# Kernel optimization log

Hardware: AMD Instinct MI355X
Metric: run time of the kernel (lower is better)

The kernel has to match this reference:

```python
import jax, jax.numpy as jnp
import numpy as np

D_MODEL = 2048
NUM_HEADS = 16
NUM_KV_HEADS = 4
HEAD_DIM = D_MODEL // NUM_HEADS  # 128
ROPE_THETA = 10000.0
BATCH = 2
SEQ = 2048


def _rotate_half(x):
    # interleaved rotate-half: pairs (x0,x1) -> (-x1, x0)
    x1 = x[..., ::2]
    x2 = x[..., 1::2]
    return jnp.stack((-x2, x1), axis=-1).reshape(x.shape)


def _rope_tables(seq_len, dtype, start_pos=0):
    inv_freq = 1.0 / (ROPE_THETA ** (jnp.arange(0, HEAD_DIM, 2, dtype=jnp.float32) / HEAD_DIM))
    positions = jnp.arange(start_pos, start_pos + seq_len, dtype=jnp.float32)
    freqs = jnp.outer(positions, inv_freq)              # [S, HD/2]
    emb = jnp.repeat(freqs, 2, axis=-1)                  # [S, HD]
    cos = jnp.cos(emb).astype(dtype)[None, None, :, :]   # [1,1,S,HD]
    sin = jnp.sin(emb).astype(dtype)[None, None, :, :]
    return cos, sin


def setup_inputs() -> dict:
    key = jax.random.key(0)
    ks = jax.random.split(key, 5)
    s = 0.02
    x = jax.random.normal(ks[0], (BATCH, SEQ, D_MODEL), dtype=jnp.float32)
    wq = jax.random.normal(ks[1], (D_MODEL, NUM_HEADS * HEAD_DIM), dtype=jnp.float32) * s
    wk = jax.random.normal(ks[2], (D_MODEL, NUM_KV_HEADS * HEAD_DIM), dtype=jnp.float32) * s
    wv = jax.random.normal(ks[3], (D_MODEL, NUM_KV_HEADS * HEAD_DIM), dtype=jnp.float32) * s
    wo = jax.random.normal(ks[4], (D_MODEL, D_MODEL), dtype=jnp.float32) * s
    return {"x": x, "wq": wq, "wk": wk, "wv": wv, "wo": wo}


def reference(x, wq, wk, wv, wo):
    batch, seq_len, _ = x.shape
    # projections (bias-free linears)
    q = (x @ wq).reshape(batch, seq_len, NUM_HEADS, HEAD_DIM).transpose(0, 2, 1, 3)
    k = (x @ wk).reshape(batch, seq_len, NUM_KV_HEADS, HEAD_DIM).transpose(0, 2, 1, 3)
    v = (x @ wv).reshape(batch, seq_len, NUM_KV_HEADS, HEAD_DIM).transpose(0, 2, 1, 3)
    # RoPE
    cos, sin = _rope_tables(seq_len, q.dtype)
    q = q * cos + _rotate_half(q) * sin
    k = k * cos + _rotate_half(k) * sin
    # GQA: duplicate KV heads
    repeats = NUM_HEADS // NUM_KV_HEADS
    k = jnp.repeat(k, repeats, axis=1)
    v = jnp.repeat(v, repeats, axis=1)
    # causal SDPA
    scale = HEAD_DIM ** -0.5
    scores = jnp.einsum('bhqd,bhkd->bhqk', q, k) * scale
    causal = jnp.tril(jnp.ones((seq_len, seq_len), dtype=bool))
    scores = jnp.where(causal[None, None, :, :], scores, -jnp.inf)
    weights = jax.nn.softmax(scores, axis=-1)
    y = jnp.einsum('bhqk,bhkd->bhqd', weights, v)
    y = y.transpose(0, 2, 1, 3).reshape(batch, seq_len, NUM_HEADS * HEAD_DIM)
    return y @ wo
```

## Files before the change

### kernel.cpp

```cpp
#include <hip/hip_runtime.h>
#include <cstdint>
#include <cstddef>

using short8 = __attribute__((ext_vector_type(8))) short;
using f32x4  = __attribute__((ext_vector_type(4))) float;
using u16x4  = __attribute__((ext_vector_type(4))) unsigned short;

#define DEV __device__ __forceinline__

DEV unsigned short f2bf(float f) {
  unsigned int u = __builtin_bit_cast(unsigned int, f);
  u += 0x7fffu + ((u >> 16) & 1u);
  return (unsigned short)(u >> 16);
}
DEV float bf2f(unsigned short h) {
  unsigned int u = ((unsigned int)h) << 16;
  return __builtin_bit_cast(float, u);
}
DEV unsigned int cvtpk_bf16(float lo, float hi) {
  unsigned int d;
  asm("v_cvt_pk_bf16_f32 %0, %1, %2" : "=v"(d) : "v"(lo), "v"(hi));
  return d;
}

#define GLL16(gp, lp)                                                          \
  __builtin_amdgcn_global_load_lds(                                            \
      (const __attribute__((address_space(1))) char*)(const char*)(gp),        \
      (__attribute__((address_space(3))) char*)(char*)(lp), 16, 0, 0)

constexpr int BATCH = 2, SEQ = 2048, DMODEL = 2048, NH = 16, NKVH = 4, DH = 128;
constexpr int MROWS = BATCH * SEQ;
constexpr int NQKV  = DMODEL + 2 * NKVH * DH;
constexpr int KOFF  = DMODEL;
constexpr int VOFF  = DMODEL + NKVH * DH;
constexpr float SM_L2 = 0.12751388158f;


__global__ void k_prep(const float* __restrict__ x, unsigned short* __restrict__ xb,
                       float* __restrict__ tc, float* __restrict__ ts) {
  int id = blockIdx.x * 256 + threadIdx.x;
  if (id < SEQ * 64) {
    int pos = id >> 6, i = id & 63;
    float freq = __expf(-(float)i * 0.14391157f);
    float ang = (float)pos * freq;
    tc[id] = cosf(ang);
    ts[id] = sinf(ang);
  }
  float4 v = ((const float4*)x)[id];
  u16x4 o = { f2bf(v.x), f2bf(v.y), f2bf(v.z), f2bf(v.w) };
  ((u16x4*)xb)[id] = o;
}

__global__ __launch_bounds__(256) void k_wtrans4(
    const float* __restrict__ wq, const float* __restrict__ wk,
    const float* __restrict__ wv, const float* __restrict__ wo,
    unsigned short* __restrict__ wT, unsigned short* __restrict__ woT) {
  __shared__ float tile[32][33];
  const int z = blockIdx.z;
  const float* src; unsigned short* dst; int N;
  if (z == 0)      { src = wq; dst = wT;                        N = 2048; }
  else if (z == 1) { src = wo; dst = woT;                       N = 2048; }
  else if (z == 2) { src = wk; dst = wT + (size_t)KOFF * 2048;  N = 512; }
  else             { src = wv; dst = wT + (size_t)VOFF * 2048;  N = 512; }
  int n0 = blockIdx.x * 32, k0 = blockIdx.y * 32;
  if (n0 >= N) return;
  int tx = threadIdx.x, ty = threadIdx.y;
  #pragma unroll
  for (int r = ty; r < 32; r += 8)
    tile[r][tx] = src[(size_t)(k0 + r) * N + n0 + tx];
  __syncthreads();
  #pragma unroll
  for (int r = ty; r < 32; r += 8)
    dst[(size_t)(n0 + r) * 2048 + k0 + tx] = f2bf(tile[tx][r]);
}

__global__ __launch_bounds__(256) void k_vtrans(const unsigned short* __restrict__ qkv,
                                                unsigned short* __restrict__ vt) {
  __shared__ unsigned short tile[32][33];
  int s0 = blockIdx.x * 32, d0 = blockIdx.y * 32;
  int bk = blockIdx.z;
  const unsigned short* src = qkv + (size_t)(bk >> 2) * SEQ * NQKV + VOFF + (bk & 3) * DH;
  unsigned short* dst = vt + ((size_t)bk * DH + d0) * SEQ + s0;
  int tx = threadIdx.x, ty = threadIdx.y;
  #pragma unroll
  for (int r = ty; r < 32; r += 8)
    tile[r][tx] = src[(size_t)(s0 + r) * NQKV + d0 + tx];
  __syncthreads();
  #pragma unroll
  for (int r = ty; r < 32; r += 8)
    dst[(size_t)r * SEQ + tx] = tile[tx][r];
}


template <int BNT, bool OUTF32, bool ROPE>
__global__ __launch_bounds__(512, 2) void k_gemm256(
    const unsigned short* __restrict__ A,
    const unsigned short* __restrict__ Bt,
    void* __restrict__ C, int M, int N, int K,
    const float* __restrict__ tc, const float* __restrict__ ts) {
  constexpr int NF = BNT / 64;
  __shared__ unsigned short As[2][256 * 64];
  __shared__ unsigned short Bs[2][BNT * 64];

  const int t = threadIdx.x, l = t & 63, w = t >> 6;
  const int rl = l & 15, kg = l >> 4;
  const int wm = w >> 2, wn = w & 3;

  const int gx = gridDim.x;
  const int nwg = gx * gridDim.y;
  const int idl = blockIdx.y * gx + blockIdx.x;
  const int swz = (idl & 7) * (nwg >> 3) + (idl >> 3);
  const int m0 = (swz / gx) * 256, n0 = (swz % gx) * BNT;

  const unsigned short* aSrc[4];
  const unsigned short* bSrc[NF];
  #pragma unroll
  for (int i = 0; i < 4; ++i) {
    int c = i * 512 + t, row = c >> 3, q = c & 7;
    aSrc[i] = A + (size_t)(m0 + row) * K + ((q ^ (row & 7)) << 3);
  }
  #pragma unroll
  for (int i = 0; i < NF; ++i) {
    int c = i * 512 + t, row = c >> 3, q = c & 7;
    bSrc[i] = Bt + (size_t)(n0 + row) * K + ((q ^ (row & 7)) << 3);
  }

  f32x4 acc[8][NF] = {};

  const int nk = K / 64;
  #pragma unroll
  for (int i = 0; i < 4; ++i) GLL16(aSrc[i], (char*)As[0] + i * 8192 + t * 16);
  #pragma unroll
  for (int i = 0; i < NF; ++i) GLL16(bSrc[i], (char*)Bs[0] + i * 8192 + t * 16);

  int cur = 0;
  for (int kt = 0; kt < nk; ++kt) {
    if (kt + 1 < nk) {
      const int off = (kt + 1) * 64;
      #pragma unroll
      for (int i = 0; i < 4; ++i)
        GLL16(aSrc[i] + off, (char*)As[cur ^ 1] + i * 8192 + t * 16);
      #pragma unroll
      for (int i = 0; i < NF; ++i)
        GLL16(bSrc[i] + off, (char*)Bs[cur ^ 1] + i * 8192 + t * 16);
      if constexpr (NF == 4)      asm volatile("s_waitcnt vmcnt(8)" ::: "memory");
      else if constexpr (NF == 3) asm volatile("s_waitcnt vmcnt(7)" ::: "memory");
      else                        asm volatile("s_waitcnt vmcnt(6)" ::: "memory");
    } else {
      asm volatile("s_waitcnt vmcnt(0)" ::: "memory");
    }
    __builtin_amdgcn_sched_barrier(0);
    __builtin_amdgcn_s_barrier();

    const unsigned short* a = As[cur];
    const unsigned short* b = Bs[cur];
    auto rdA = [&](int mf, int ks) {
      int row = wm * 128 + mf * 16 + rl;
      return *(const short8*)&a[row * 64 + (((ks * 4 + kg) ^ (row & 7)) << 3)];
    };
    auto rdB = [&](int nf, int ks) {
      int row = wn * (BNT / 4) + nf * 16 + rl;
      return *(const short8*)&b[row * 64 + (((ks * 4 + kg) ^ (row & 7)) << 3)];
    };

    short8 aF[4][2], bF[NF][2];
    #pragma unroll
    for (int mi = 0; mi < 4; ++mi)
      #pragma unroll
      for (int ks = 0; ks < 2; ++ks) aF[mi][ks] = rdA(mi, ks);
    #pragma unroll
    for (int j = 0; j < NF; ++j) {
      #pragma unroll
      for (int ks = 0; ks < 2; ++ks) bF[j][ks] = rdB(j, ks);
      __builtin_amdgcn_s_setprio(1);
      #pragma unroll
      for (int mi = 0; mi < 4; ++mi)
        #pragma unroll
        for (int ks = 0; ks < 2; ++ks)
          acc[mi][j] = __builtin_amdgcn_mfma_f32_16x16x32_bf16(aF[mi][ks], bF[j][ks], acc[mi][j], 0, 0, 0);
      __builtin_amdgcn_s_setprio(0);
    }
    #pragma unroll
    for (int mi = 0; mi < 4; ++mi)
      #pragma unroll
      for (int ks = 0; ks < 2; ++ks) aF[mi][ks] = rdA(4 + mi, ks);
    #pragma unroll
    for (int j = 0; j < NF; ++j) {
      __builtin_amdgcn_s_setprio(1);
      #pragma unroll
      for (int mi = 0; mi < 4; ++mi)
        #pragma unroll
        for (int ks = 0; ks < 2; ++ks)
          acc[4 + mi][j] = __builtin_amdgcn_mfma_f32_16x16x32_bf16(aF[mi][ks], bF[j][ks], acc[4 + mi][j], 0, 0, 0);
      __builtin_amdgcn_s_setprio(0);
    }

    __builtin_amdgcn_s_barrier();
    cur ^= 1;
  }

  #pragma unroll
  for (int mf = 0; mf < 8; ++mf) {
    #pragma unroll
    for (int nf = 0; nf < NF; ++nf) {
      const int row0 = m0 + wm * 128 + mf * 16 + kg * 4;
      const int colb = n0 + wn * (BNT / 4) + nf * 16;
      const int col = colb + rl;
      if constexpr (ROPE) {
        if (colb < VOFF) {
          const int dd = (col & 127) >> 1;
          const float sgn = (col & 1) ? 1.0f : -1.0f;
          const float qs = (colb < KOFF) ? SM_L2 : 1.0f;
          #pragma unroll
          for (int r = 0; r < 4; ++r) {
            const int s = (row0 + r) & (SEQ - 1);
            const float c = tc[s * 64 + dd], sn = ts[s * 64 + dd];
            const float xv = acc[mf][nf][r];
            const float xp = __shfl_xor(xv, 1);
            acc[mf][nf][r] = (xv * c + sgn * xp * sn) * qs;
          }
        }
      }
      #pragma unroll
      for (int r = 0; r < 4; ++r) {
        if constexpr (OUTF32)
          ((float*)C)[(size_t)(row0 + r) * N + col] = acc[mf][nf][r];
        else
          ((unsigned short*)C)[(size_t)(row0 + r) * N + col] = f2bf(acc[mf][nf][r]);
      }
    }
  }
}


constexpr int QB = 128, KB = 64;
constexpr float THR = 8.0f;

__global__ __launch_bounds__(512, 4) void k_attn(const unsigned short* __restrict__ qkv,
                                                 const unsigned short* __restrict__ vt,
                                                 unsigned short* __restrict__ obuf) {
  __shared__ unsigned short Ks[2][KB * DH];
  __shared__ unsigned short Vs[2][DH * KB];
  __shared__ unsigned short Pw[8][16 * 64];

  const int t = threadIdx.x, l = t & 63, w = t >> 6;
  const int rl = l & 15, kg = l >> 4;

  const int id = blockIdx.x;
  const int b = id >> 8;
  const int u = id & 255;
  const int h = u >> 4;
  const int qtr = u & 15;
  const int qt = b ? (15 - qtr) : qtr;
  const int q0 = qt * QB;
  const int kvh = h >> 2;

  const unsigned short* qbase = qkv + (size_t)b * SEQ * NQKV;
  const unsigned short* kbase = qbase + KOFF + kvh * DH;
  const unsigned short* vtb = vt + (size_t)(b * NKVH + kvh) * DH * SEQ;

  const unsigned short* kp[2];
  const unsigned short* vp[2];
  #pragma unroll
  for (int i = 0; i < 2; ++i) {
    int c = i * 512 + t;
    int krow = c >> 4, kq = c & 15;
    kp[i] = kbase + (size_t)krow * NQKV + ((kq ^ (krow & 7)) << 3);
    int vrow = c >> 3, vq = c & 7;
    vp[i] = vtb + (size_t)vrow * SEQ + ((vq ^ (vrow & 7)) << 3);
  }

  const int qw0 = q0 + w * 16;

  short8 qF[4];
  {
    const size_t qr = (size_t)(qw0 + rl) * NQKV + h * DH;
    #pragma unroll
    for (int ks = 0; ks < 4; ++ks)
      qF[ks] = *(const short8*)(qbase + qr + ks * 32 + kg * 8);
  }

  f32x4 Oc[8] = {};
  float mr = -3e38f, lr = 0.f;

  char* pwB = (char*)Pw[w] + rl * 128;
  const int pkey = (rl & 7) << 4;
  const int nt = q0 / KB + 2;

  #pragma unroll
  for (int i = 0; i < 2; ++i) {
    GLL16(kp[i], (char*)Ks[0] + w * 1024 + i * 8192);
    GLL16(vp[i], (char*)Vs[0] + w * 1024 + i * 8192);
  }

  int cur = 0;
  for (int tt = 0; tt < nt; ++tt) {
    const int kv0 = tt * KB;
    const bool more = (tt + 1 < nt);
    if (more) {
      #pragma unroll
      for (int i = 0; i < 2; ++i) {
        GLL16(kp[i] + (size_t)(kv0 + KB) * NQKV, (char*)Ks[cur ^ 1] + w * 1024 + i * 8192);
        GLL16(vp[i] + (kv0 + KB),               (char*)Vs[cur ^ 1] + w * 1024 + i * 8192);
      }
      asm volatile("s_waitcnt vmcnt(4)" ::: "memory");
    } else {
      asm volatile("s_waitcnt vmcnt(0)" ::: "memory");
    }
    __builtin_amdgcn_sched_barrier(0);
    __builtin_amdgcn_s_barrier();

    if (kv0 < qw0 + 16) {
      const unsigned short* KsC = Ks[cur];
      const unsigned short* VsC = Vs[cur];

      f32x4 St[4] = {};
      __builtin_amdgcn_s_setprio(1);
      #pragma unroll
      for (int n = 0; n < 4; ++n) {
        const int kr = n * 16 + rl;
        #pragma unroll
        for (int ks = 0; ks < 4; ++ks) {
          short8 kF = *(const short8*)&KsC[kr * DH + (((ks * 4 + kg) ^ (kr & 7)) << 3)];
          St[n] = __builtin_amdgcn_mfma_f32_16x16x32_bf16(kF, qF[ks], St[n], 0, 0, 0);
        }
      }
      __builtin_amdgcn_s_setprio(0);

      float mx = -3e38f;
      const bool diag = (kv0 + KB - 1) > qw0;
      if (diag) {
        const int thr = qw0 + rl - kv0;
        #pragma unroll
        for (int n = 0; n < 4; ++n)
          #pragma unroll
          for (int r = 0; r < 4; ++r) {
            float s = St[n][r];
            if (n * 16 + kg * 4 + r > thr) s = -3e38f;
            St[n][r] = s;
            mx = fmaxf(mx, s);
          }
      } else {
        #pragma unroll
        for (int n = 0; n < 4; ++n)
          #pragma unroll
          for (int r = 0; r < 4; ++r) mx = fmaxf(mx, St[n][r]);
      }
      mx = fmaxf(mx, __shfl_xor(mx, 16));
      mx = fmaxf(mx, __shfl_xor(mx, 32));

      if (__any(mx > mr + THR)) {
        const float mnew = fmaxf(mr, mx);
        const float sf = exp2f(mr - mnew);
        mr = mnew;
        lr *= sf;
        float sfv[4];
        #pragma unroll
        for (int r = 0; r < 4; ++r) sfv[r] = __shfl(sf, kg * 4 + r, 16);
        #pragma unroll
        for (int c = 0; c < 8; ++c)
          #pragma unroll
          for (int r = 0; r < 4; ++r) Oc[c][r] *= sfv[r];
      }

      float rs = 0.f;
      #pragma unroll
      for (int n = 0; n < 4; ++n) {
        float e0 = exp2f(St[n][0] - mr);
        float e1 = exp2f(St[n][1] - mr);
        float e2 = exp2f(St[n][2] - mr);
        float e3 = exp2f(St[n][3] - mr);
        rs += (e0 + e1) + (e2 + e3);
        uint2 d;
        d.x = cvtpk_bf16(e0, e1);
        d.y = cvtpk_bf16(e2, e3);
        *(uint2*)(pwB + ((n * 32 + kg * 8) ^ pkey)) = d;
      }
      rs += __shfl_xor(rs, 16);
      rs += __shfl_xor(rs, 32);
      lr += rs;

      short8 pF[2];
      #pragma unroll
      for (int ks2 = 0; ks2 < 2; ++ks2)
        pF[ks2] = *(const short8*)(pwB + ((ks2 * 64 + kg * 16) ^ pkey));
      __builtin_amdgcn_s_setprio(1);
      #pragma unroll
      for (int c = 0; c < 8; ++c) {
        const int vr = c * 16 + rl;
        #pragma unroll
        for (int ks2 = 0; ks2 < 2; ++ks2) {
          short8 vF = *(const short8*)&VsC[vr * KB + (((ks2 * 4 + kg) ^ (vr & 7)) << 3)];
          Oc[c] = __builtin_amdgcn_mfma_f32_16x16x32_bf16(pF[ks2], vF, Oc[c], 0, 0, 0);
        }
      }
      __builtin_amdgcn_s_setprio(0);
    }

    __builtin_amdgcn_s_barrier();
    cur ^= 1;
  }

  const float linv = 1.0f / lr;
  float inv[4];
  #pragma unroll
  for (int r = 0; r < 4; ++r) inv[r] = __shfl(linv, kg * 4 + r, 16);
  #pragma unroll
  for (int c = 0; c < 8; ++c)
    #pragma unroll
    for (int r = 0; r < 4; ++r) {
      int row = b * SEQ + qw0 + kg * 4 + r;
      obuf[(size_t)row * DMODEL + h * DH + c * 16 + rl] = f2bf(Oc[c][r] * inv[r]);
    }
}


extern "C" void kernel_launch(void* const* d_in, const int* in_sizes, int n_in,
                              void* d_out, int out_size, void* d_ws, size_t ws_size,
                              hipStream_t stream) {
  const float* x  = (const float*)d_in[0];
  const float* wq = (const float*)d_in[1];
  const float* wk = (const float*)d_in[2];
  const float* wv = (const float*)d_in[3];
  const float* wo = (const float*)d_in[4];
  float* out = (float*)d_out;

  unsigned short* xb  = (unsigned short*)d_ws;
  unsigned short* wT  = xb  + (size_t)MROWS * DMODEL;
  unsigned short* woT = wT  + (size_t)NQKV * DMODEL;
  unsigned short* qkv = woT + (size_t)DMODEL * DMODEL;
  unsigned short* ob  = qkv + (size_t)MROWS * NQKV;
  float* tc = (float*)(ob + (size_t)MROWS * DMODEL);
  float* ts = tc + SEQ * 64;
  unsigned short* vtG = wT;

  k_prep<<<dim3(MROWS * DMODEL / 4 / 256), dim3(256), 0, stream>>>(x, xb, tc, ts);
  k_wtrans4<<<dim3(64, 64, 4), dim3(32, 8), 0, stream>>>(wq, wk, wv, wo, wT, woT);

  k_gemm256<192, false, true><<<dim3(NQKV / 192, MROWS / 256), dim3(512), 0, stream>>>(
      xb, wT, qkv, MROWS, NQKV, DMODEL, tc, ts);
  k_vtrans<<<dim3(SEQ / 32, DH / 32, BATCH * NKVH), dim3(32, 8), 0, stream>>>(qkv, vtG);
  k_attn<<<dim3(512), dim3(512), 0, stream>>>(qkv, vtG, ob);
  k_gemm256<128, true, false><<<dim3(DMODEL / 128, MROWS / 256), dim3(512), 0, stream>>>(
      ob, woT, out, MROWS, DMODEL, DMODEL, nullptr, nullptr);
}
```

Baseline: 212.3 us.

## Switch attention to 32x32x16 MFMA with register-resident P via permlane32 swap

Reworks the attention inner loop to use 32x32x16 bf16 MFMAs. Each pair of waves now shares a 32-row query tile, and each wave in the pair computes one 64-wide half of the head dimension. The softmax probabilities stay in registers and are rearranged with v_permlane32_swap into the B-operand layout, so the per-wave LDS scratch buffer and its write/read round-trip are removed. Scale factors become per-lane and the output is stored as packed 4-element bf16 writes. In exchange, the QK^T scores are computed twice (once by each wave in a pair), and the larger fragments raise register pressure under the 512x4 launch bounds.

```diff
diff --git a/kernel.cpp b/kernel.cpp
--- a/kernel.cpp
+++ b/kernel.cpp
@@ -4,6 +4,7 @@
 
 using short8 = __attribute__((ext_vector_type(8))) short;
 using f32x4  = __attribute__((ext_vector_type(4))) float;
+using f32x16 = __attribute__((ext_vector_type(16))) float;
 using u16x4  = __attribute__((ext_vector_type(4))) unsigned short;
 
 #define DEV __device__ __forceinline__
@@ -241,10 +242,12 @@
                                                  unsigned short* __restrict__ obuf) {
   __shared__ unsigned short Ks[2][KB * DH];
   __shared__ unsigned short Vs[2][DH * KB];
-  __shared__ unsigned short Pw[8][16 * 64];
 
   const int t = threadIdx.x, l = t & 63, w = t >> 6;
-  const int rl = l & 15, kg = l >> 4;
+  const int ql = l & 31;
+  const int hi = l >> 5;
+  const int wq = w >> 1;
+  const int dhalf = (w & 1) * 64;
 
   const int id = blockIdx.x;
   const int b = id >> 8;
@@ -270,21 +273,19 @@
     vp[i] = vtb + (size_t)vrow * SEQ + ((vq ^ (vrow & 7)) << 3);
   }
 
-  const int qw0 = q0 + w * 16;
-
-  short8 qF[4];
+  const int qw0 = q0 + wq * 32;
+
+  short8 qF[8];
   {
-    const size_t qr = (size_t)(qw0 + rl) * NQKV + h * DH;
-    #pragma unroll
-    for (int ks = 0; ks < 4; ++ks)
-      qF[ks] = *(const short8*)(qbase + qr + ks * 32 + kg * 8);
-  }
-
-  f32x4 Oc[8] = {};
+    const size_t qr = (size_t)(qw0 + ql) * NQKV + h * DH;
+    #pragma unroll
+    for (int ks = 0; ks < 8; ++ks)
+      qF[ks] = *(const short8*)(qbase + qr + ks * 16 + hi * 8);
+  }
+
+  f32x16 Oc[2] = {};
   float mr = -3e38f, lr = 0.f;
 
-  char* pwB = (char*)Pw[w] + rl * 128;
-  const int pkey = (rl & 7) << 4;
   const int nt = q0 / KB + 2;
 
   #pragma unroll
@@ -310,19 +311,19 @@
     __builtin_amdgcn_sched_barrier(0);
     __builtin_amdgcn_s_barrier();
 
-    if (kv0 < qw0 + 16) {
+    if (kv0 < qw0 + 32) {
       const unsigned short* KsC = Ks[cur];
       const unsigned short* VsC = Vs[cur];
 
-      f32x4 St[4] = {};
+      f32x16 St[2] = {};
       __builtin_amdgcn_s_setprio(1);
       #pragma unroll
-      for (int n = 0; n < 4; ++n) {
-        const int kr = n * 16 + rl;
-        #pragma unroll
-        for (int ks = 0; ks < 4; ++ks) {
-          short8 kF = *(const short8*)&KsC[kr * DH + (((ks * 4 + kg) ^ (kr & 7)) << 3)];
-          St[n] = __builtin_amdgcn_mfma_f32_16x16x32_bf16(kF, qF[ks], St[n], 0, 0, 0);
+      for (int c = 0; c < 2; ++c) {
+        const int krow = c * 32 + ql;
+        #pragma unroll
+        for (int ks = 0; ks < 8; ++ks) {
+          short8 kF = *(const short8*)&KsC[krow * DH + (((ks * 2 + hi) ^ (krow & 7)) << 3)];
+          St[c] = __builtin_amdgcn_mfma_f32_32x32x16_bf16(kF, qF[ks], St[c], 0, 0, 0);
         }
       }
       __builtin_amdgcn_s_setprio(0);
@@ -330,23 +331,23 @@
       float mx = -3e38f;
       const bool diag = (kv0 + KB - 1) > qw0;
       if (diag) {
-        const int thr = qw0 + rl - kv0;
-        #pragma unroll
-        for (int n = 0; n < 4; ++n)
+        const int thr = qw0 + ql - kv0;
+        #pragma unroll
+        for (int c = 0; c < 2; ++c)
           #pragma unroll
-          for (int r = 0; r < 4; ++r) {
-            float s = St[n][r];
-            if (n * 16 + kg * 4 + r > thr) s = -3e38f;
-            St[n][r] = s;
+          for (int r = 0; r < 16; ++r) {
+            const int kvl = c * 32 + (r & 3) + 8 * (r >> 2) + 4 * hi;
+            float s = St[c][r];
+            if (kvl > thr) s = -3e38f;
+            St[c][r] = s;
             mx = fmaxf(mx, s);
           }
       } else {
         #pragma unroll
-        for (int n = 0; n < 4; ++n)
+        for (int c = 0; c < 2; ++c)
           #pragma unroll
-          for (int r = 0; r < 4; ++r) mx = fmaxf(mx, St[n][r]);
-      }
-      mx = fmaxf(mx, __shfl_xor(mx, 16));
+          for (int r = 0; r < 16; ++r) mx = fmaxf(mx, St[c][r]);
+      }
       mx = fmaxf(mx, __shfl_xor(mx, 32));
 
       if (__any(mx > mr + THR)) {
@@ -354,44 +355,47 @@
         const float sf = exp2f(mr - mnew);
         mr = mnew;
         lr *= sf;
-        float sfv[4];
-        #pragma unroll
-        for (int r = 0; r < 4; ++r) sfv[r] = __shfl(sf, kg * 4 + r, 16);
-        #pragma unroll
-        for (int c = 0; c < 8; ++c)
+        #pragma unroll
+        for (int cc = 0; cc < 2; ++cc)
           #pragma unroll
-          for (int r = 0; r < 4; ++r) Oc[c][r] *= sfv[r];
+          for (int r = 0; r < 16; ++r) Oc[cc][r] *= sf;
       }
 
       float rs = 0.f;
       #pragma unroll
-      for (int n = 0; n < 4; ++n) {
-        float e0 = exp2f(St[n][0] - mr);
-        float e1 = exp2f(St[n][1] - mr);
-        float e2 = exp2f(St[n][2] - mr);
-        float e3 = exp2f(St[n][3] - mr);
-        rs += (e0 + e1) + (e2 + e3);
-        uint2 d;
-        d.x = cvtpk_bf16(e0, e1);
-        d.y = cvtpk_bf16(e2, e3);
-        *(uint2*)(pwB + ((n * 32 + kg * 8) ^ pkey)) = d;
-      }
-      rs += __shfl_xor(rs, 16);
+      for (int c = 0; c < 2; ++c)
+        #pragma unroll
+        for (int r = 0; r < 16; ++r) {
+          float e = exp2f(St[c][r] - mr);
+          St[c][r] = e;
+          rs += e;
+        }
       rs += __shfl_xor(rs, 32);
       lr += rs;
 
-      short8 pF[2];
-      #pragma unroll
-      for (int ks2 = 0; ks2 < 2; ++ks2)
-        pF[ks2] = *(const short8*)(pwB + ((ks2 * 64 + kg * 16) ^ pkey));
+      short8 pB[4];
+      #pragma unroll
+      for (int c = 0; c < 2; ++c)
+        #pragma unroll
+        for (int s = 0; s < 2; ++s) {
+          unsigned int X0 = cvtpk_bf16(St[c][s * 8 + 0], St[c][s * 8 + 1]);
+          unsigned int X1 = cvtpk_bf16(St[c][s * 8 + 2], St[c][s * 8 + 3]);
+          unsigned int X2 = cvtpk_bf16(St[c][s * 8 + 4], St[c][s * 8 + 5]);
+          unsigned int X3 = cvtpk_bf16(St[c][s * 8 + 6], St[c][s * 8 + 7]);
+          asm("v_permlane32_swap_b32 %0, %1" : "+v"(X0), "+v"(X2));
+          asm("v_permlane32_swap_b32 %0, %1" : "+v"(X1), "+v"(X3));
+          uint4 uw = { X0, X1, X2, X3 };
+          pB[c * 2 + s] = __builtin_bit_cast(short8, uw);
+        }
+
       __builtin_amdgcn_s_setprio(1);
       #pragma unroll
-      for (int c = 0; c < 8; ++c) {
-        const int vr = c * 16 + rl;
-        #pragma unroll
-        for (int ks2 = 0; ks2 < 2; ++ks2) {
-          short8 vF = *(const short8*)&VsC[vr * KB + (((ks2 * 4 + kg) ^ (vr & 7)) << 3)];
-          Oc[c] = __builtin_amdgcn_mfma_f32_16x16x32_bf16(pF[ks2], vF, Oc[c], 0, 0, 0);
+      for (int cc = 0; cc < 2; ++cc) {
+        const int vrow = dhalf + cc * 32 + ql;
+        #pragma unroll
+        for (int ks2 = 0; ks2 < 4; ++ks2) {
+          short8 vF = *(const short8*)&VsC[vrow * KB + (((ks2 * 2 + hi) ^ (vrow & 7)) << 3)];
+          Oc[cc] = __builtin_amdgcn_mfma_f32_32x32x16_bf16(vF, pB[ks2], Oc[cc], 0, 0, 0);
         }
       }
       __builtin_amdgcn_s_setprio(0);
@@ -402,15 +406,15 @@
   }
 
   const float linv = 1.0f / lr;
-  float inv[4];
-  #pragma unroll
-  for (int r = 0; r < 4; ++r) inv[r] = __shfl(linv, kg * 4 + r, 16);
-  #pragma unroll
-  for (int c = 0; c < 8; ++c)
-    #pragma unroll
-    for (int r = 0; r < 4; ++r) {
-      int row = b * SEQ + qw0 + kg * 4 + r;
-      obuf[(size_t)row * DMODEL + h * DH + c * 16 + rl] = f2bf(Oc[c][r] * inv[r]);
+  const size_t rowb = (size_t)(b * SEQ + qw0 + ql) * DMODEL + h * DH + dhalf;
+  #pragma unroll
+  for (int cc = 0; cc < 2; ++cc)
+    #pragma unroll
+    for (int rq = 0; rq < 4; ++rq) {
+      uint2 dwords;
+      dwords.x = cvtpk_bf16(Oc[cc][rq * 4 + 0] * linv, Oc[cc][rq * 4 + 1] * linv);
+      dwords.y = cvtpk_bf16(Oc[cc][rq * 4 + 2] * linv, Oc[cc][rq * 4 + 3] * linv);
+      *(uint2*)&obuf[rowb + cc * 32 + 8 * rq + 4 * hi] = dwords;
     }
 }
 
```

Measured after the change: 274.1 us. 29.1% more time.
